# Performance work log

Hardware: AMD Instinct MI355X
Metric: run time of the kernel (lower is better)

Reference implementation:

```python
import jax, jax.numpy as jnp
import numpy as np

L, B, D = 2048, 8, 1024
EPS = 1e-5  # torch LayerNorm default


def setup_inputs() -> dict:
    key = jax.random.key(0)
    k1, k2 = jax.random.split(key)
    x = jax.random.normal(k1, (L, B, D), dtype=jnp.float32)
    c = jnp.zeros((B, D), dtype=jnp.float32)
    W_ufr = 0.02 * jax.random.normal(k2, (3 * D, D), dtype=jnp.float32)
    ln_gamma = jnp.ones((D,), dtype=jnp.float32)
    ln_beta = jnp.zeros((D,), dtype=jnp.float32)
    return {"x": x, "c": c, "W_ufr": W_ufr, "ln_gamma": ln_gamma, "ln_beta": ln_beta}


def reference(x, c, W_ufr, ln_gamma, ln_beta):
    # LayerNorm over last dim
    mean = jnp.mean(x, axis=-1, keepdims=True)
    var = jnp.mean(jnp.square(x - mean), axis=-1, keepdims=True)
    x_norm = (x - mean) * jax.lax.rsqrt(var + EPS) * ln_gamma + ln_beta

    # Linear (no bias): [L,B,D] @ [D,3D]
    ufr = jnp.einsum('lbd,ed->lbe', x_norm, W_ufr)
    u, f, r = jnp.split(ufr, 3, axis=-1)
    f_gate = jax.nn.sigmoid(f)
    r_gate = jax.nn.sigmoid(r)

    # Sequential recurrence: c_t = f_t * c_{t-1} + (1 - f_t) * u_t
    def step(c_prev, fu):
        f_t, u_t = fu
        c_t = f_t * c_prev + (1.0 - f_t) * u_t
        return c_t, c_t

    last_c, c_stack = jax.lax.scan(step, c, (f_gate, u))

    hs = r_gate * jnp.tanh(c_stack) + (1.0 - r_gate) * x_norm
    return x + hs, last_c
```

## Files before the change

kernel.cpp:

```cpp
#include <hip/hip_runtime.h>
#include <hip/hip_bf16.h>
#include <stdint.h>

#define L_DIM 2048
#define B_DIM 8
#define D_DIM 1024
#define M_DIM (L_DIM * B_DIM)
#define N_DIM (3 * D_DIM)
#define K_DIM D_DIM
#define CH    (B_DIM * D_DIM)
#define EPSLN 1e-5f
#define NC 128
#define CL (L_DIM / NC)

#define BM 256
#define BN 256
#define BK 64
#define NT (K_DIM / BK)
#define GX (N_DIM / BN)
#define GY (M_DIM / BM)
#define NWG (GX * GY)

typedef __attribute__((ext_vector_type(8))) short short8;
typedef __attribute__((ext_vector_type(4))) float floatx4;

static __device__ __forceinline__ float bf16_lo(unsigned int p) {
    union { unsigned int u; float f; } v; v.u = p << 16; return v.f;
}
static __device__ __forceinline__ float bf16_hi(unsigned int p) {
    union { unsigned int u; float f; } v; v.u = p & 0xffff0000u; return v.f;
}
static __device__ __forceinline__ unsigned short f32_to_bf16(float f) {
    union { float f; unsigned int u; } v;
    v.f = f;
    unsigned int u = v.u;
    u += 0x7fffu + ((u >> 16) & 1u);
    return (unsigned short)(u >> 16);
}
static __device__ __forceinline__ float sigmoidf_fast(float v) {
    return 1.0f / (1.0f + __expf(-v));
}
static __device__ __forceinline__ float tanhf_fast(float c) {
    return 1.0f - 2.0f / (1.0f + __expf(2.0f * c));
}

static __device__ __forceinline__ void async16(const void* g, void* l) {
    __builtin_amdgcn_global_load_lds(
        (const __attribute__((address_space(1))) unsigned int*)g,
        (__attribute__((address_space(3))) unsigned int*)l,
        16, 0, 0);
}

__global__ __launch_bounds__(256) void ln_kernel(const float* __restrict__ x,
                                                 const float* __restrict__ gamma,
                                                 const float* __restrict__ beta,
                                                 unsigned short* __restrict__ xn,
                                                 float* __restrict__ meanOut,
                                                 float* __restrict__ rstdOut) {
    const int row = blockIdx.x;
    const int tid = threadIdx.x;
    const float4* xr = (const float4*)(x + (size_t)row * D_DIM);
    float4 v = xr[tid];
    float s  = v.x + v.y + v.z + v.w;
    float s2 = v.x * v.x + v.y * v.y + v.z * v.z + v.w * v.w;
    #pragma unroll
    for (int o = 32; o > 0; o >>= 1) {
        s  += __shfl_xor(s, o, 64);
        s2 += __shfl_xor(s2, o, 64);
    }
    __shared__ float red[8];
    const int wid = tid >> 6;
    if ((tid & 63) == 0) { red[wid] = s; red[4 + wid] = s2; }
    __syncthreads();
    s  = red[0] + red[1] + red[2] + red[3];
    s2 = red[4] + red[5] + red[6] + red[7];
    const float mean = s * (1.0f / D_DIM);
    const float var  = s2 * (1.0f / D_DIM) - mean * mean;
    const float rstd = rsqrtf(var + EPSLN);
    if (tid == 0) { meanOut[row] = mean; rstdOut[row] = rstd; }
    const int col = tid * 4;
    const float4 g = *(const float4*)(gamma + col);
    const float4 b = *(const float4*)(beta + col);
    unsigned short o0 = f32_to_bf16((v.x - mean) * rstd * g.x + b.x);
    unsigned short o1 = f32_to_bf16((v.y - mean) * rstd * g.y + b.y);
    unsigned short o2 = f32_to_bf16((v.z - mean) * rstd * g.z + b.z);
    unsigned short o3 = f32_to_bf16((v.w - mean) * rstd * g.w + b.w);
    uint2 packed;
    packed.x = (unsigned int)o0 | ((unsigned int)o1 << 16);
    packed.y = (unsigned int)o2 | ((unsigned int)o3 << 16);
    *(uint2*)(xn + (size_t)row * D_DIM + col) = packed;
}

__global__ __launch_bounds__(256) void wconv_kernel(const float* __restrict__ W,
                                                    unsigned short* __restrict__ Wb) {
    const size_t i = ((size_t)blockIdx.x * 256 + threadIdx.x) * 4;
    float4 v = *(const float4*)(W + i);
    uint2 packed;
    packed.x = (unsigned int)f32_to_bf16(v.x) | ((unsigned int)f32_to_bf16(v.y) << 16);
    packed.y = (unsigned int)f32_to_bf16(v.z) | ((unsigned int)f32_to_bf16(v.w) << 16);
    *(uint2*)(Wb + i) = packed;
}

__global__ __launch_bounds__(512, 2) void gemm_kernel(const unsigned short* __restrict__ A,
                                                      const unsigned short* __restrict__ W,
                                                      unsigned short* __restrict__ u,
                                                      unsigned short* __restrict__ f,
                                                      unsigned short* __restrict__ r) {
    __shared__ __align__(16) unsigned short ldsA[2][BM * BK];
    __shared__ __align__(16) unsigned short ldsB[2][BM * BK];

    const int tid  = threadIdx.x;
    const int wave = tid >> 6;
    const int lane = tid & 63;
    const int quad = lane >> 4;
    const int l16  = lane & 15;
    const int wr   = wave >> 2;
    const int wc   = wave & 3;

    const int orig = blockIdx.y * GX + blockIdx.x;
    const int swz  = (orig & 7) * (NWG / 8) + (orig >> 3);
    const int tx   = swz % GX;
    const int ty   = swz / GX;
    const int m0   = ty * BM;
    const int n0   = tx * BN;

    const int rS = tid >> 3;
    const int kS = ((tid & 7) ^ (rS & 7)) * 8;
    const unsigned short* gA = A + (size_t)(m0 + rS) * K_DIM + kS;
    const unsigned short* gB = W + (size_t)(n0 + rS) * K_DIM + kS;

    const int px     = l16 & 7;
    const int p0_8   = (quad ^ px) * 8;
    const int p1_8   = ((quad + 4) ^ px) * 8;
    const int l16_64 = l16 * 64;
    const int wr4096 = wr * 4096;
    const int wc2048 = wc * 2048;

    floatx4 acc[2][2][4][2] = {};
    short8 a[4][2];
    short8 b[2][2][2];

#define STAGE_A(B_, KT_, H_) do { \
    async16(gA + (size_t)((H_) * 128) * K_DIM + (size_t)(KT_) * 64, \
            &ldsA[B_][(H_) * 8192 + (size_t)tid * 8]); \
    async16(gA + (size_t)((H_) * 128 + 64) * K_DIM + (size_t)(KT_) * 64, \
            &ldsA[B_][(H_) * 8192 + 4096 + (size_t)tid * 8]); \
} while (0)

#define STAGE_B(B_, KT_, H_) do { \
    async16(gB + (size_t)((H_) * 128) * K_DIM + (size_t)(KT_) * 64, \
            &ldsB[B_][(H_) * 8192 + (size_t)tid * 8]); \
    async16(gB + (size_t)((H_) * 128 + 64) * K_DIM + (size_t)(KT_) * 64, \
            &ldsB[B_][(H_) * 8192 + 4096 + (size_t)tid * 8]); \
} while (0)

#define RD_A(MH_) do { \
    const unsigned short* pa_ = &ldsA[buf][(MH_) * 8192 + wr4096 + l16_64]; \
    _Pragma("unroll") \
    for (int i_ = 0; i_ < 4; i_++) { \
        a[i_][0] = *(const short8*)(pa_ + i_ * 1024 + p0_8); \
        a[i_][1] = *(const short8*)(pa_ + i_ * 1024 + p1_8); \
    } \
} while (0)

#define RD_B(NH_) do { \
    const unsigned short* pb_ = &ldsB[buf][(NH_) * 8192 + wc2048 + l16_64]; \
    _Pragma("unroll") \
    for (int j_ = 0; j_ < 2; j_++) { \
        b[NH_][j_][0] = *(const short8*)(pb_ + j_ * 1024 + p0_8); \
        b[NH_][j_][1] = *(const short8*)(pb_ + j_ * 1024 + p1_8); \
    } \
} while (0)

#define PHASE(RDSTMT, STAGESTMT, MH_, NH_, VM_) do { \
    RDSTMT; \
    STAGESTMT; \
    __builtin_amdgcn_s_barrier(); \
    asm volatile("s_waitcnt lgkmcnt(0)" ::: "memory"); \
    __builtin_amdgcn_sched_barrier(0); \
    __builtin_amdgcn_s_setprio(1); \
    _Pragma("unroll") \
    for (int i_ = 0; i_ < 4; i_++) { \
        _Pragma("unroll") \
        for (int j_ = 0; j_ < 2; j_++) { \
            acc[MH_][NH_][i_][j_] = __builtin_amdgcn_mfma_f32_16x16x32_bf16( \
                a[i_][0], b[NH_][j_][0], acc[MH_][NH_][i_][j_], 0, 0, 0); \
            acc[MH_][NH_][i_][j_] = __builtin_amdgcn_mfma_f32_16x16x32_bf16( \
                a[i_][1], b[NH_][j_][1], acc[MH_][NH_][i_][j_], 0, 0, 0); \
        } \
    } \
    __builtin_amdgcn_s_setprio(0); \
    __builtin_amdgcn_sched_barrier(0); \
    asm volatile("s_waitcnt vmcnt(" VM_ ")" ::: "memory"); \
    __builtin_amdgcn_s_barrier(); \
    asm volatile("" ::: "memory"); \
} while (0)

    STAGE_A(0, 0, 0); STAGE_A(0, 0, 1);
    STAGE_B(0, 0, 0); STAGE_B(0, 0, 1);
    asm volatile("s_waitcnt vmcnt(0)" ::: "memory");
    __builtin_amdgcn_s_barrier();
    asm volatile("" ::: "memory");

    for (int kt = 0; kt < NT - 1; ++kt) {
        const int buf  = kt & 1;
        const int nbuf = buf ^ 1;
        PHASE({ RD_A(0); RD_B(0); }, STAGE_A(nbuf, kt + 1, 0), 0, 0, "4");
        PHASE(RD_B(1),               STAGE_B(nbuf, kt + 1, 0), 0, 1, "4");
        PHASE(RD_A(1),               STAGE_B(nbuf, kt + 1, 1), 1, 1, "4");
        PHASE((void)0,               STAGE_A(nbuf, kt + 1, 1), 1, 0, "4");
    }

    {
        const int buf = (NT - 1) & 1;
        PHASE({ RD_A(0); RD_B(0); }, (void)0, 0, 0, "2");
        PHASE(RD_B(1),               (void)0, 0, 1, "0");
        PHASE(RD_A(1),               (void)0, 1, 1, "0");
        PHASE((void)0,               (void)0, 1, 0, "0");
    }

#undef PHASE
#undef RD_A
#undef RD_B
#undef STAGE_A
#undef STAGE_B

    const int region = n0 >> 10;
    const int nnb = n0 & 1023;
    unsigned short* dst = (region == 0) ? u : ((region == 1) ? f : r);
    const bool sig = (region != 0);
    #pragma unroll
    for (int mh = 0; mh < 2; mh++) {
        #pragma unroll
        for (int nh = 0; nh < 2; nh++) {
            #pragma unroll
            for (int i = 0; i < 4; i++) {
                #pragma unroll
                for (int j = 0; j < 2; j++) {
                    #pragma unroll
                    for (int t = 0; t < 4; t++) {
                        const int gm = m0 + mh * 128 + wr * 64 + i * 16 + quad * 4 + t;
                        const int nn = nnb + nh * 128 + wc * 32 + j * 16 + l16;
                        float v = acc[mh][nh][i][j][t];
                        if (sig) v = sigmoidf_fast(v);
                        dst[(size_t)gm * D_DIM + nn] = f32_to_bf16(v);
                    }
                }
            }
        }
    }
}

__global__ __launch_bounds__(256) void scan_reduce(const unsigned short* __restrict__ f,
                                                   const unsigned short* __restrict__ u,
                                                   float* __restrict__ Ac,
                                                   float* __restrict__ bc) {
    const int ch2   = (blockIdx.x * 256 + threadIdx.x) * 2;
    const int chunk = blockIdx.y;
    const size_t base = (size_t)chunk * CL * CH + ch2;
    float A0 = 1.0f, b0 = 0.0f, A1 = 1.0f, b1 = 0.0f;
    #pragma unroll
    for (int i = 0; i < CL; i++) {
        const size_t idx = base + (size_t)i * CH;
        const unsigned int fp = *(const unsigned int*)(f + idx);
        const unsigned int up = *(const unsigned int*)(u + idx);
        const float f0 = bf16_lo(fp), f1 = bf16_hi(fp);
        const float u0 = bf16_lo(up), u1 = bf16_hi(up);
        b0 = f0 * (b0 - u0) + u0;
        b1 = f1 * (b1 - u1) + u1;
        A0 *= f0;
        A1 *= f1;
    }
    *(float2*)(Ac + chunk * CH + ch2) = make_float2(A0, A1);
    *(float2*)(bc + chunk * CH + ch2) = make_float2(b0, b1);
}

__global__ __launch_bounds__(256) void scan_spine(const float* __restrict__ Ac,
                                                  const float* __restrict__ bc,
                                                  const float* __restrict__ c0,
                                                  float* __restrict__ cst) {
    const int ch = blockIdx.x * 256 + threadIdx.x;
    float c = c0[ch];
    #pragma unroll 16
    for (int j = 0; j < NC; j++) {
        cst[j * CH + ch] = c;
        c = Ac[j * CH + ch] * c + bc[j * CH + ch];
    }
}

__global__ __launch_bounds__(256) void scan_apply(const unsigned short* __restrict__ f,
                                                  const unsigned short* __restrict__ u,
                                                  const unsigned short* __restrict__ r,
                                                  const float* __restrict__ x,
                                                  const float* __restrict__ meanIn,
                                                  const float* __restrict__ rstdIn,
                                                  const float* __restrict__ gamma,
                                                  const float* __restrict__ beta,
                                                  const float* __restrict__ cst,
                                                  float* __restrict__ out,
                                                  float* __restrict__ lastc) {
    const int ch2   = (blockIdx.x * 256 + threadIdx.x) * 2;
    const int chunk = blockIdx.y;
    const int bidx  = ch2 >> 10;
    const int d     = ch2 & 1023;
    const float2 g  = *(const float2*)(gamma + d);
    const float2 be = *(const float2*)(beta + d);
    const size_t base = (size_t)chunk * CL * CH + ch2;
    float2 cc = *(const float2*)(cst + chunk * CH + ch2);
    float c0v = cc.x, c1v = cc.y;
    #pragma unroll 4
    for (int i = 0; i < CL; i++) {
        const int rowLB = (chunk * CL + i) * B_DIM + bidx;
        const float mu = meanIn[rowLB];
        const float rs = rstdIn[rowLB];
        const size_t idx = base + (size_t)i * CH;
        const unsigned int fp = *(const unsigned int*)(f + idx);
        const unsigned int up = *(const unsigned int*)(u + idx);
        const unsigned int rp = *(const unsigned int*)(r + idx);
        const float2 xv = *(const float2*)(x + idx);
        const float f0 = bf16_lo(fp), f1 = bf16_hi(fp);
        const float u0 = bf16_lo(up), u1 = bf16_hi(up);
        c0v = f0 * (c0v - u0) + u0;
        c1v = f1 * (c1v - u1) + u1;
        const float r0 = bf16_lo(rp), r1 = bf16_hi(rp);
        const float n0 = (xv.x - mu) * rs * g.x + be.x;
        const float n1 = (xv.y - mu) * rs * g.y + be.y;
        float2 o;
        o.x = xv.x + r0 * tanhf_fast(c0v) + (1.0f - r0) * n0;
        o.y = xv.y + r1 * tanhf_fast(c1v) + (1.0f - r1) * n1;
        *(float2*)(out + idx) = o;
    }
    if (chunk == NC - 1) *(float2*)(lastc + ch2) = make_float2(c0v, c1v);
}

extern "C" void kernel_launch(void* const* d_in, const int* in_sizes, int n_in,
                              void* d_out, int out_size, void* d_ws, size_t ws_size,
                              hipStream_t stream) {
    const float* x     = (const float*)d_in[0];
    const float* c0    = (const float*)d_in[1];
    const float* W     = (const float*)d_in[2];
    const float* gamma = (const float*)d_in[3];
    const float* beta  = (const float*)d_in[4];

    float* out   = (float*)d_out;
    float* lastc = out + (size_t)M_DIM * D_DIM;

    char* ws = (char*)d_ws;
    unsigned short* xn = (unsigned short*)ws;  ws += (size_t)M_DIM * K_DIM * 2;
    unsigned short* Wb = (unsigned short*)ws;  ws += (size_t)N_DIM * K_DIM * 2;
    unsigned short* u  = (unsigned short*)ws;  ws += (size_t)M_DIM * D_DIM * 2;
    unsigned short* f  = (unsigned short*)ws;  ws += (size_t)M_DIM * D_DIM * 2;
    unsigned short* r  = (unsigned short*)ws;  ws += (size_t)M_DIM * D_DIM * 2;
    float* meanBuf = (float*)ws;               ws += (size_t)M_DIM * 4;
    float* rstdBuf = (float*)ws;               ws += (size_t)M_DIM * 4;
    float* Ac  = (float*)ws;                   ws += (size_t)NC * CH * 4;
    float* bc  = (float*)ws;                   ws += (size_t)NC * CH * 4;
    float* cst = (float*)ws;                   ws += (size_t)NC * CH * 4;

    ln_kernel<<<M_DIM, 256, 0, stream>>>(x, gamma, beta, xn, meanBuf, rstdBuf);
    wconv_kernel<<<(N_DIM * K_DIM) / 1024, 256, 0, stream>>>(W, Wb);
    gemm_kernel<<<dim3(GX, GY), 512, 0, stream>>>(xn, Wb, u, f, r);
    scan_reduce<<<dim3(CH / 512, NC), 256, 0, stream>>>(f, u, Ac, bc);
    scan_spine<<<CH / 256, 256, 0, stream>>>(Ac, bc, c0, cst);
    scan_apply<<<dim3(CH / 512, NC), 256, 0, stream>>>(f, u, r, x, meanBuf, rstdBuf,
                                                       gamma, beta, cst, out, lastc);
}
```

Baseline: 299.7 us.

## Restructure GEMM main loop barriers and staging order to cut sync points

```diff
diff --git a/kernel.cpp b/kernel.cpp
--- a/kernel.cpp
+++ b/kernel.cpp
@@ -172,12 +172,13 @@
     } \
 } while (0)
 
-#define PHASE(RDSTMT, STAGESTMT, MH_, NH_, VM_) do { \
-    RDSTMT; \
-    STAGESTMT; \
-    __builtin_amdgcn_s_barrier(); \
-    asm volatile("s_waitcnt lgkmcnt(0)" ::: "memory"); \
-    __builtin_amdgcn_sched_barrier(0); \
+#define BARR __builtin_amdgcn_s_barrier()
+#define VMW4 asm volatile("s_waitcnt vmcnt(4)" ::: "memory")
+#define VMW0 asm volatile("s_waitcnt vmcnt(0)" ::: "memory")
+#define LGKM0 do { asm volatile("s_waitcnt lgkmcnt(0)" ::: "memory"); \
+                   __builtin_amdgcn_sched_barrier(0); } while (0)
+
+#define MFMA_Q(MH_, NH_) do { \
     __builtin_amdgcn_s_setprio(1); \
     _Pragma("unroll") \
     for (int i_ = 0; i_ < 4; i_++) { \
@@ -191,35 +192,50 @@
     } \
     __builtin_amdgcn_s_setprio(0); \
     __builtin_amdgcn_sched_barrier(0); \
-    asm volatile("s_waitcnt vmcnt(" VM_ ")" ::: "memory"); \
-    __builtin_amdgcn_s_barrier(); \
-    asm volatile("" ::: "memory"); \
-} while (0)
-
-    STAGE_A(0, 0, 0); STAGE_A(0, 0, 1);
-    STAGE_B(0, 0, 0); STAGE_B(0, 0, 1);
-    asm volatile("s_waitcnt vmcnt(0)" ::: "memory");
-    __builtin_amdgcn_s_barrier();
-    asm volatile("" ::: "memory");
+} while (0)
+
+    STAGE_A(0, 0, 0); STAGE_B(0, 0, 0);
+    STAGE_A(0, 0, 1); STAGE_B(0, 0, 1);
+    VMW4;
+    BARR;
 
     for (int kt = 0; kt < NT - 1; ++kt) {
         const int buf  = kt & 1;
         const int nbuf = buf ^ 1;
-        PHASE({ RD_A(0); RD_B(0); }, STAGE_A(nbuf, kt + 1, 0), 0, 0, "4");
-        PHASE(RD_B(1),               STAGE_B(nbuf, kt + 1, 0), 0, 1, "4");
-        PHASE(RD_A(1),               STAGE_B(nbuf, kt + 1, 1), 1, 1, "4");
-        PHASE((void)0,               STAGE_A(nbuf, kt + 1, 1), 1, 0, "4");
+        RD_A(0); RD_B(0);
+        STAGE_A(nbuf, kt + 1, 0); STAGE_B(nbuf, kt + 1, 0);
+        VMW4; BARR; LGKM0;
+        MFMA_Q(0, 0);
+        RD_B(1);
+        STAGE_B(nbuf, kt + 1, 1); STAGE_A(nbuf, kt + 1, 1);
+        BARR; LGKM0;
+        MFMA_Q(0, 1);
+        RD_A(1);
+        BARR; LGKM0;
+        MFMA_Q(1, 1);
+        VMW4; BARR;
+        MFMA_Q(1, 0);
     }
 
     {
         const int buf = (NT - 1) & 1;
-        PHASE({ RD_A(0); RD_B(0); }, (void)0, 0, 0, "2");
-        PHASE(RD_B(1),               (void)0, 0, 1, "0");
-        PHASE(RD_A(1),               (void)0, 1, 1, "0");
-        PHASE((void)0,               (void)0, 1, 0, "0");
-    }
-
-#undef PHASE
+        RD_A(0); RD_B(0);
+        VMW0; BARR; LGKM0;
+        MFMA_Q(0, 0);
+        RD_B(1);
+        BARR; LGKM0;
+        MFMA_Q(0, 1);
+        RD_A(1);
+        BARR; LGKM0;
+        MFMA_Q(1, 1);
+        MFMA_Q(1, 0);
+    }
+
+#undef MFMA_Q
+#undef LGKM0
+#undef VMW0
+#undef VMW4
+#undef BARR
 #undef RD_A
 #undef RD_B
 #undef STAGE_A
```

After: 289.3 us. 1.04x faster.
